# Performance work log

Measured on AMD Instinct MI355X. Metric: run time of the kernel, lower is better.

## Reference

```python
import math
import jax, jax.numpy as jnp
import numpy as np

B, N, E, H, DPOS = 64, 196, 768, 16, 3
DH = E // H


def rel_pos(num_patches):
    # deterministic relative-position encodings [N, N, 3] = (dx, dy, d^2)
    v = int(math.isqrt(num_patches))
    ind = jnp.arange(v)[None, :] - jnp.arange(v)[:, None]          # [v, v]
    indx = jnp.tile(ind, (v, v))                                    # [N, N]
    indy = jnp.repeat(jnp.repeat(ind, v, axis=0), v, axis=1)       # [N, N]
    indd = indx ** 2 + indy ** 2
    return jnp.stack([indx, indy, indd], axis=-1).astype(jnp.float32)


def setup_inputs() -> dict:
    key = jax.random.key(0)
    ks = jax.random.split(key, 9)
    std = 0.02  # trunc_normal std used by the module's init
    return {
        "q": jax.random.normal(ks[0], (B, N, E), jnp.float32),
        "k": jax.random.normal(ks[1], (B, N, E), jnp.float32),
        "v": jax.random.normal(ks[2], (B, N, E), jnp.float32),
        "mask": jnp.ones((B, 1, N, N), jnp.bool_),
        "Wq": jax.random.normal(ks[3], (E, E), jnp.float32) * std,
        "Wk": jax.random.normal(ks[4], (E, E), jnp.float32) * std,
        "Wv": jax.random.normal(ks[5], (E, E), jnp.float32) * std,
        "Wo": jax.random.normal(ks[6], (E, E), jnp.float32) * std,
        "bo": jnp.zeros((E,), jnp.float32),
        "Wpos": jax.random.normal(ks[7], (H, DPOS), jnp.float32) * std,
        "bpos": jnp.zeros((H,), jnp.float32),
        "gating": jnp.ones((H,), jnp.float32),
    }


def reference(q, k, v, mask, Wq, Wk, Wv, Wo, bo, Wpos, bpos, gating):
    b, n, _ = q.shape

    def heads(x, W):  # [b, n, E] -> [b, H, n, DH]
        return (x @ W.T).reshape(b, n, H, DH).transpose(0, 2, 1, 3)

    Q, K, V = heads(q, Wq), heads(k, Wk), heads(v, Wv)

    energy = jnp.einsum('bhqd,bhkd->bhqk', Q, K) / math.sqrt(DH)
    energy = jnp.where(mask, energy, -jnp.inf)
    content = jax.nn.softmax(energy, axis=-1)                      # [b, H, n, n]

    rel = rel_pos(n)                                               # [n, n, 3]
    pos = jnp.einsum('qkp,hp->hqk', rel, Wpos) + bpos[:, None, None]
    pos = jax.nn.softmax(pos, axis=-1)[None]                       # [1, H, n, n]

    g = jax.nn.sigmoid(gating)[None, :, None, None]
    score = (1.0 - g) * content + g * pos
    score = score / jnp.sum(score, axis=-1, keepdims=True)

    attn = jnp.einsum('bhqk,bhkd->bhqd', score, V)
    out = attn.transpose(0, 2, 1, 3).reshape(b, n, E) @ Wo.T + bo
    return out
```

## Files before the change

kernel.cpp:

```cpp
#include <hip/hip_runtime.h>
#include <hip/hip_bf16.h>

#define BB 64
#define NN 196
#define EE 768
#define HH 16
#define DHH 48

typedef short bf16x8 __attribute__((ext_vector_type(8)));
typedef float f32x4 __attribute__((ext_vector_type(4)));
typedef unsigned short u16;
typedef unsigned short u16x8 __attribute__((ext_vector_type(8)));
typedef unsigned int u32;

static __device__ __forceinline__ u16 f2bf(float f) {
  union { float f; u32 u; } un; un.f = f;
  u32 u = un.u;
  u32 r = (u + 0x7fffu + ((u >> 16) & 1u)) >> 16;
  return (u16)r;
}

static __device__ __forceinline__ u16 f2bf_hw(float f) {
  __hip_bfloat16 h = __float2bfloat16(f);
  return __builtin_bit_cast(u16, h);
}

#define GLOAD16(GP, LP)                                                        \
  __builtin_amdgcn_global_load_lds(                                            \
      (const __attribute__((address_space(1))) void*)(GP),                     \
      (__attribute__((address_space(3))) void*)(LP), 16, 0, 0)

static __device__ __forceinline__ int xcd_swz(int bid, int nwg) {
  int q = nwg >> 3, r = nwg & 7;
  int xcd = bid & 7, i = bid >> 3;
  return (xcd < r ? xcd * (q + 1) : r * (q + 1) + (xcd - r) * q) + i;
}

__global__ __launch_bounds__(64) void pos_kernel(const float* __restrict__ Wpos,
                                                 const float* __restrict__ bpos,
                                                 float* __restrict__ pos) {
  int bid = blockIdx.x;
  int h = bid / NN, q = bid % NN;
  int lane = threadIdx.x;
  float w0 = Wpos[h * 3 + 0], w1 = Wpos[h * 3 + 1], w2 = Wpos[h * 3 + 2];
  float bb = bpos[h];
  int qx = q % 14, qy = q / 14;
  float e[4];
  float mx = -1e30f;
#pragma unroll
  for (int i = 0; i < 4; ++i) {
    int k = lane + 64 * i;
    float val = -1e30f;
    if (k < NN) {
      int kx = k % 14, ky = k / 14;
      float dx = (float)(kx - qx), dy = (float)(ky - qy);
      val = w0 * dx + w1 * dy + w2 * (dx * dx + dy * dy) + bb;
    }
    e[i] = val;
    mx = fmaxf(mx, val);
  }
#pragma unroll
  for (int off = 1; off < 64; off <<= 1) mx = fmaxf(mx, __shfl_xor(mx, off));
  float s = 0.f;
#pragma unroll
  for (int i = 0; i < 4; ++i) {
    int k = lane + 64 * i;
    float p = (k < NN) ? expf(e[i] - mx) : 0.f;
    e[i] = p;
    s += p;
  }
#pragma unroll
  for (int off = 1; off < 64; off <<= 1) s += __shfl_xor(s, off);
  float inv = 1.f / s;
#pragma unroll
  for (int i = 0; i < 4; ++i) {
    int k = lane + 64 * i;
    if (k < NN) pos[(size_t)h * NN * NN + (size_t)q * NN + k] = e[i] * inv;
  }
}

__global__ __launch_bounds__(256) void cvtw_kernel(const float* __restrict__ W0,
                                                   const float* __restrict__ W1,
                                                   const float* __restrict__ W2,
                                                   const float* __restrict__ W3,
                                                   u16* __restrict__ out) {
  const float* Ws[4] = {W0, W1, W2, W3};
  int mat = blockIdx.y;
  const float* src = Ws[mat];
  int idx = blockIdx.x * 256 + threadIdx.x;
  float4 f = ((const float4*)src)[idx];
  short4 s;
  s.x = (short)f2bf_hw(f.x);
  s.y = (short)f2bf_hw(f.y);
  s.z = (short)f2bf_hw(f.z);
  s.w = (short)f2bf_hw(f.w);
  *(short4*)(out + (size_t)mat * EE * EE + (size_t)idx * 4) = s;
}

__global__ __launch_bounds__(256) void cvtx_kernel(const float* __restrict__ q,
                                                   const float* __restrict__ k,
                                                   const float* __restrict__ v,
                                                   u16* __restrict__ qb,
                                                   u16* __restrict__ kb,
                                                   u16* __restrict__ vb) {
  const float* srcs[3] = {q, k, v};
  u16* dsts[3] = {qb, kb, vb};
  const float* src = srcs[blockIdx.y];
  u16* dst = dsts[blockIdx.y];
#pragma unroll
  for (int c = 0; c < 4; ++c) {
    size_t idx = (size_t)blockIdx.x * 1024 + c * 256 + threadIdx.x;
    float4 f = ((const float4*)src)[idx];
    short4 s;
    s.x = (short)f2bf_hw(f.x);
    s.y = (short)f2bf_hw(f.y);
    s.z = (short)f2bf_hw(f.z);
    s.w = (short)f2bf_hw(f.w);
    ((short4*)dst)[idx] = s;
  }
}

template <bool OUT_F32>
static __device__ __forceinline__ void gemm_body(const u16* __restrict__ Aptr,
                                                 const u16* __restrict__ Wb,
                                                 void* __restrict__ Yptr,
                                                 const float* __restrict__ bias,
                                                 int m0, int n0) {
  __shared__ u16 As[3][128 * 32];
  __shared__ u16 Bs[3][128 * 32];
  const int tid = threadIdx.x;
  const int lane = tid & 63, wid = tid >> 6;
  const int wm = wid >> 1, wn = wid & 1;
  const int r16 = lane & 15, g4 = lane >> 4;
  f32x4 acc[4][4];
#pragma unroll
  for (int i = 0; i < 4; ++i)
#pragma unroll
    for (int j = 0; j < 4; ++j) acc[i][j] = (f32x4){0.f, 0.f, 0.f, 0.f};

  auto gloadA = [&](int b, int k0) {
#pragma unroll
    for (int c = 0; c < 2; ++c) {
      int s = c * 256 + tid;
      GLOAD16(Aptr + (size_t)(m0 + (s >> 2)) * EE + k0 + (s & 3) * 8,
              &As[b][s * 8]);
    }
  };
  auto gloadB = [&](int b, int k0) {
#pragma unroll
    for (int c = 0; c < 2; ++c) {
      int s = c * 256 + tid;
      GLOAD16(Wb + (size_t)(n0 + (s >> 2)) * EE + k0 + (s & 3) * 8,
              &Bs[b][s * 8]);
    }
  };

  gloadA(0, 0);  gloadB(0, 0);
  gloadA(1, 32); gloadB(1, 32);
  asm volatile("s_waitcnt vmcnt(4)" ::: "memory");
  asm volatile("s_barrier" ::: "memory");

  for (int t = 0; t < 24; ++t) {
    const int cb = t % 3;
    const int sb = (t + 2) % 3;
    const bool st = t < 22;
    if (st) {
      gloadA(sb, (t + 2) * 32);
      gloadB(sb, (t + 2) * 32);
    }
    bf16x8 af[4], bf[4];
#pragma unroll
    for (int i = 0; i < 4; ++i)
      af[i] = *(const bf16x8*)&As[cb][(wm * 64 + i * 16 + r16) * 32 + g4 * 8];
#pragma unroll
    for (int j = 0; j < 4; ++j)
      bf[j] = *(const bf16x8*)&Bs[cb][(wn * 64 + j * 16 + r16) * 32 + g4 * 8];
#pragma unroll
    for (int i = 0; i < 4; ++i)
#pragma unroll
      for (int j = 0; j < 4; ++j)
        acc[i][j] = __builtin_amdgcn_mfma_f32_16x16x32_bf16(af[i], bf[j], acc[i][j], 0, 0, 0);
    if (st)
      asm volatile("s_waitcnt vmcnt(4)" ::: "memory");
    else
      asm volatile("s_waitcnt vmcnt(0)" ::: "memory");
    asm volatile("s_barrier" ::: "memory");
  }

#pragma unroll
  for (int i = 0; i < 4; ++i) {
    int row = m0 + wm * 64 + i * 16 + g4 * 4;
#pragma unroll
    for (int j = 0; j < 4; ++j) {
      int col = n0 + wn * 64 + j * 16 + r16;
#pragma unroll
      for (int v = 0; v < 4; ++v) {
        float val = acc[i][j][v];
        if (OUT_F32)
          ((float*)Yptr)[(size_t)(row + v) * EE + col] = val + bias[col];
        else
          ((u16*)Yptr)[(size_t)(row + v) * EE + col] = f2bf(val);
      }
    }
  }
}

__global__ __launch_bounds__(256) void qkv_gemm(const u16* __restrict__ qb,
                                                const u16* __restrict__ kb,
                                                const u16* __restrict__ vb,
                                                const u16* __restrict__ Wqb,
                                                const u16* __restrict__ Wkb,
                                                const u16* __restrict__ Wvb,
                                                u16* __restrict__ Qp,
                                                u16* __restrict__ Kp,
                                                u16* __restrict__ Vp) {
  int sid = xcd_swz(blockIdx.x, 3 * 98 * 6);
  int z = sid / 588, rem = sid % 588;
  int m0 = (rem / 6) * 128, n0 = (rem % 6) * 128;
  const u16* A = (z == 0) ? qb : (z == 1) ? kb : vb;
  const u16* W = (z == 0) ? Wqb : (z == 1) ? Wkb : Wvb;
  u16* Y = (z == 0) ? Qp : (z == 1) ? Kp : Vp;
  gemm_body<false>(A, W, Y, nullptr, m0, n0);
}

__global__ __launch_bounds__(256) void out_gemm(const u16* __restrict__ ctx,
                                                const u16* __restrict__ Wob,
                                                float* __restrict__ out,
                                                const float* __restrict__ bo) {
  int sid = xcd_swz(blockIdx.x, 98 * 6);
  int m0 = (sid / 6) * 128, n0 = (sid % 6) * 128;
  gemm_body<true>(ctx, Wob, out, bo, m0, n0);
}

__global__ __launch_bounds__(512) void attn_kernel(const u16* __restrict__ Qp,
                                                   const u16* __restrict__ Kp,
                                                   const u16* __restrict__ Vp,
                                                   const float* __restrict__ pos,
                                                   const float* __restrict__ gating,
                                                   u16* __restrict__ ctx) {
  __shared__ u16 Qs[208 * 72];
  __shared__ u16 Ks[208 * 72];
  __shared__ u16 Vt[48 * 232];
  __shared__ u16 sc[8][16 * 232];
  int bh = blockIdx.x;
  int b = bh >> 4, h = bh & 15;
  int tid = threadIdx.x;
  {
    u32* z = (u32*)&Qs[0];
    for (int i = tid; i < (208 * 72) / 2; i += 512) z[i] = 0u;
    z = (u32*)&Ks[0];
    for (int i = tid; i < (208 * 72) / 2; i += 512) z[i] = 0u;
    z = (u32*)&Vt[0];
    for (int i = tid; i < (48 * 232) / 2; i += 512) z[i] = 0u;
  }
  __syncthreads();
  const u16* Qb = Qp + (size_t)b * NN * EE + h * DHH;
  const u16* Kb = Kp + (size_t)b * NN * EE + h * DHH;
  const u16* Vb = Vp + (size_t)b * NN * EE + h * DHH;
  for (int c = tid; c < NN * 12; c += 512) {
    int row = c / 12, k4 = (c % 12) * 4;
    short4 v = *(const short4*)(Qb + (size_t)row * EE + k4);
    *(short4*)&Qs[row * 72 + k4] = v;
  }
  for (int c = tid; c < NN * 12; c += 512) {
    int row = c / 12, k4 = (c % 12) * 4;
    short4 v = *(const short4*)(Kb + (size_t)row * EE + k4);
    *(short4*)&Ks[row * 72 + k4] = v;
  }
  for (int c = tid; c < NN * 12; c += 512) {
    int key = c / 12, d4 = (c % 12) * 4;
    short4 v = *(const short4*)(Vb + (size_t)key * EE + d4);
    Vt[(d4 + 0) * 232 + key] = (u16)v.x;
    Vt[(d4 + 1) * 232 + key] = (u16)v.y;
    Vt[(d4 + 2) * 232 + key] = (u16)v.z;
    Vt[(d4 + 3) * 232 + key] = (u16)v.w;
  }
  __syncthreads();

  int wid = tid >> 6, lane = tid & 63;
  int r16 = lane & 15, g4 = lane >> 4;
  float g = 1.f / (1.f + expf(-gating[h]));
  float omg = 1.f - g;
  u16* scw = &sc[wid][0];
  const float scale = 0.14433756729740643f;
  const float* posh = pos + (size_t)h * NN * NN;

  for (int rt = wid; rt < 13; rt += 8) {
    int q0 = rt * 16;
    bf16x8 aQ0 = *(const bf16x8*)&Qs[(q0 + r16) * 72 + g4 * 8];
    bf16x8 aQ1 = *(const bf16x8*)&Qs[(q0 + r16) * 72 + 32 + g4 * 8];
    f32x4 e[13];
#pragma unroll
    for (int ct = 0; ct < 13; ++ct) {
      bf16x8 b0 = *(const bf16x8*)&Ks[(ct * 16 + r16) * 72 + g4 * 8];
      bf16x8 b1 = *(const bf16x8*)&Ks[(ct * 16 + r16) * 72 + 32 + g4 * 8];
      f32x4 t = (f32x4){0.f, 0.f, 0.f, 0.f};
      t = __builtin_amdgcn_mfma_f32_16x16x32_bf16(aQ0, b0, t, 0, 0, 0);
      t = __builtin_amdgcn_mfma_f32_16x16x32_bf16(aQ1, b1, t, 0, 0, 0);
      e[ct] = t;
    }
    float mx[4] = {-1e30f, -1e30f, -1e30f, -1e30f};
#pragma unroll
    for (int ct = 0; ct < 13; ++ct) {
      int cix = ct * 16 + r16;
      bool valid = cix < NN;
#pragma unroll
      for (int v = 0; v < 4; ++v) {
        float ev = e[ct][v] * scale;
        ev = valid ? ev : -1e30f;
        e[ct][v] = ev;
        mx[v] = fmaxf(mx[v], ev);
      }
    }
#pragma unroll
    for (int v = 0; v < 4; ++v)
#pragma unroll
      for (int off = 1; off < 16; off <<= 1) mx[v] = fmaxf(mx[v], __shfl_xor(mx[v], off));
    float sm[4] = {0.f, 0.f, 0.f, 0.f};
#pragma unroll
    for (int ct = 0; ct < 13; ++ct)
#pragma unroll
      for (int v = 0; v < 4; ++v) {
        float p = __expf(e[ct][v] - mx[v]);
        e[ct][v] = p;
        sm[v] += p;
      }
#pragma unroll
    for (int v = 0; v < 4; ++v)
#pragma unroll
      for (int off = 1; off < 16; off <<= 1) sm[v] += __shfl_xor(sm[v], off);
    float inv[4];
#pragma unroll
    for (int v = 0; v < 4; ++v) inv[v] = 1.f / sm[v];
    int qg[4];
#pragma unroll
    for (int v = 0; v < 4; ++v) qg[v] = q0 + g4 * 4 + v;
    float t2[4] = {0.f, 0.f, 0.f, 0.f};
#pragma unroll
    for (int ct = 0; ct < 13; ++ct) {
      int cix = ct * 16 + r16;
      bool valid = cix < NN;
#pragma unroll
      for (int v = 0; v < 4; ++v) {
        float content = e[ct][v] * inv[v];
        float pv = 0.f;
        if (valid && qg[v] < NN) pv = posh[(size_t)qg[v] * NN + cix];
        float s = omg * content + g * pv;
        e[ct][v] = s;
        t2[v] += s;
      }
    }
#pragma unroll
    for (int v = 0; v < 4; ++v)
#pragma unroll
      for (int off = 1; off < 16; off <<= 1) t2[v] += __shfl_xor(t2[v], off);
    float inv2[4];
#pragma unroll
    for (int v = 0; v < 4; ++v) inv2[v] = 1.f / t2[v];
#pragma unroll
    for (int ct = 0; ct < 14; ++ct)
#pragma unroll
      for (int v = 0; v < 4; ++v) {
        float s = (ct < 13) ? e[ct][v] * inv2[v] : 0.f;
        scw[(g4 * 4 + v) * 232 + ct * 16 + r16] = f2bf(s);
      }
    asm volatile("s_waitcnt lgkmcnt(0)" ::: "memory");
#pragma unroll
    for (int dt = 0; dt < 3; ++dt) {
      f32x4 pv = (f32x4){0.f, 0.f, 0.f, 0.f};
#pragma unroll
      for (int kt = 0; kt < 7; ++kt) {
        bf16x8 aS = *(const bf16x8*)&scw[r16 * 232 + kt * 32 + g4 * 8];
        bf16x8 bV = *(const bf16x8*)&Vt[(dt * 16 + r16) * 232 + kt * 32 + g4 * 8];
        pv = __builtin_amdgcn_mfma_f32_16x16x32_bf16(aS, bV, pv, 0, 0, 0);
      }
#pragma unroll
      for (int v = 0; v < 4; ++v) {
        if (qg[v] < NN)
          ctx[((size_t)b * NN + qg[v]) * EE + h * DHH + dt * 16 + r16] = f2bf(pv[v]);
      }
    }
  }
}

extern "C" void kernel_launch(void* const* d_in, const int* in_sizes, int n_in,
                              void* d_out, int out_size, void* d_ws, size_t ws_size,
                              hipStream_t stream) {
  const float* q = (const float*)d_in[0];
  const float* k = (const float*)d_in[1];
  const float* v = (const float*)d_in[2];
  const float* Wq = (const float*)d_in[4];
  const float* Wk = (const float*)d_in[5];
  const float* Wv = (const float*)d_in[6];
  const float* Wo = (const float*)d_in[7];
  const float* bo = (const float*)d_in[8];
  const float* Wpos = (const float*)d_in[9];
  const float* bpos = (const float*)d_in[10];
  const float* gating = (const float*)d_in[11];
  float* out = (float*)d_out;

  char* ws = (char*)d_ws;
  const size_t elems = (size_t)BB * NN * EE;
  u16* Qp = (u16*)ws;
  u16* Kp = Qp + elems;
  u16* Vp = Kp + elems;
  u16* ctx = Vp + elems;
  float* pos = (float*)(ws + 4 * elems * sizeof(u16));
  u16* Wqb = (u16*)(ws + 4 * elems * sizeof(u16) + (size_t)HH * NN * NN * sizeof(float));
  u16* Wkb = Wqb + (size_t)EE * EE;
  u16* Wvb = Wkb + (size_t)EE * EE;
  u16* Wob = Wvb + (size_t)EE * EE;
  u16* qb = (u16*)d_out;
  u16* kb = qb + elems;
  u16* vb = ctx;

  hipLaunchKernelGGL(pos_kernel, dim3(HH * NN), dim3(64), 0, stream, Wpos, bpos, pos);
  hipLaunchKernelGGL(cvtw_kernel, dim3(EE * EE / 4 / 256, 4), dim3(256), 0, stream,
                     Wq, Wk, Wv, Wo, Wqb);
  hipLaunchKernelGGL(cvtx_kernel, dim3(2352, 3), dim3(256), 0, stream,
                     q, k, v, qb, kb, vb);

  hipLaunchKernelGGL(qkv_gemm, dim3(3 * 98 * 6), dim3(256), 0, stream,
                     qb, kb, vb, Wqb, Wkb, Wvb, Qp, Kp, Vp);

  hipLaunchKernelGGL(attn_kernel, dim3(BB * HH), dim3(512), 0, stream,
                     Qp, Kp, Vp, pos, gating, ctx);

  hipLaunchKernelGGL(out_gemm, dim3(98 * 6), dim3(256), 0, stream,
                     ctx, Wob, out, bo);
}
```

Baseline: 222.8 us.

## Restructure attention kernel to 256 threads, register-resident Q, and drop renormalization

The attention kernel moves from 512 to 256 threads per block with launch bounds allowing two blocks per CU. Q fragments now load straight from global memory into registers, so the Q shared-memory tile and its zeroing go away and each block uses less LDS. The second row-sum normalization is removed on the reasoning that the mixed score already sums to one, and the omg factor is folded into the softmax reciprocal. Score rows are converted with the hardware bf16 conversion and the S fragments are loaded once and reused across the three V tiles. Each wave now handles up to four row tiles, so the block runs longer and register pressure rises.

```diff
diff --git a/kernel.cpp b/kernel.cpp
--- a/kernel.cpp
+++ b/kernel.cpp
@@ -232,42 +232,51 @@
   gemm_body<true>(ctx, Wob, out, bo, m0, n0);
 }
 
-__global__ __launch_bounds__(512) void attn_kernel(const u16* __restrict__ Qp,
-                                                   const u16* __restrict__ Kp,
-                                                   const u16* __restrict__ Vp,
-                                                   const float* __restrict__ pos,
-                                                   const float* __restrict__ gating,
-                                                   u16* __restrict__ ctx) {
-  __shared__ u16 Qs[208 * 72];
+__global__ __launch_bounds__(256, 2) void attn_kernel(const u16* __restrict__ Qp,
+                                                      const u16* __restrict__ Kp,
+                                                      const u16* __restrict__ Vp,
+                                                      const float* __restrict__ pos,
+                                                      const float* __restrict__ gating,
+                                                      u16* __restrict__ ctx) {
   __shared__ u16 Ks[208 * 72];
   __shared__ u16 Vt[48 * 232];
-  __shared__ u16 sc[8][16 * 232];
+  __shared__ u16 sc[4][16 * 224];
   int bh = blockIdx.x;
   int b = bh >> 4, h = bh & 15;
   int tid = threadIdx.x;
-  {
-    u32* z = (u32*)&Qs[0];
-    for (int i = tid; i < (208 * 72) / 2; i += 512) z[i] = 0u;
-    z = (u32*)&Ks[0];
-    for (int i = tid; i < (208 * 72) / 2; i += 512) z[i] = 0u;
-    z = (u32*)&Vt[0];
-    for (int i = tid; i < (48 * 232) / 2; i += 512) z[i] = 0u;
-  }
-  __syncthreads();
+  int wid = tid >> 6, lane = tid & 63;
+  int r16 = lane & 15, g4 = lane >> 4;
+
   const u16* Qb = Qp + (size_t)b * NN * EE + h * DHH;
   const u16* Kb = Kp + (size_t)b * NN * EE + h * DHH;
   const u16* Vb = Vp + (size_t)b * NN * EE + h * DHH;
-  for (int c = tid; c < NN * 12; c += 512) {
-    int row = c / 12, k4 = (c % 12) * 4;
-    short4 v = *(const short4*)(Qb + (size_t)row * EE + k4);
-    *(short4*)&Qs[row * 72 + k4] = v;
-  }
-  for (int c = tid; c < NN * 12; c += 512) {
+
+  bf16x8 aQ0[4], aQ1[4];
+#pragma unroll
+  for (int i = 0; i < 4; ++i) {
+    int rt = wid + 4 * i;
+    if (rt < 13) {
+      int qrow = rt * 16 + r16;
+      if (qrow > NN - 1) qrow = NN - 1;
+      const u16* qp = Qb + (size_t)qrow * EE;
+      aQ0[i] = *(const bf16x8*)(qp + g4 * 8);
+      aQ1[i] = *(const bf16x8*)(qp + 32 + g4 * 8);
+    }
+  }
+
+  {
+    u32* z = (u32*)&Ks[0];
+    for (int i = tid; i < (208 * 72) / 2; i += 256) z[i] = 0u;
+    z = (u32*)&Vt[0];
+    for (int i = tid; i < (48 * 232) / 2; i += 256) z[i] = 0u;
+  }
+  __syncthreads();
+  for (int c = tid; c < NN * 12; c += 256) {
     int row = c / 12, k4 = (c % 12) * 4;
     short4 v = *(const short4*)(Kb + (size_t)row * EE + k4);
     *(short4*)&Ks[row * 72 + k4] = v;
   }
-  for (int c = tid; c < NN * 12; c += 512) {
+  for (int c = tid; c < NN * 12; c += 256) {
     int key = c / 12, d4 = (c % 12) * 4;
     short4 v = *(const short4*)(Vb + (size_t)key * EE + d4);
     Vt[(d4 + 0) * 232 + key] = (u16)v.x;
@@ -277,107 +286,95 @@
   }
   __syncthreads();
 
-  int wid = tid >> 6, lane = tid & 63;
-  int r16 = lane & 15, g4 = lane >> 4;
   float g = 1.f / (1.f + expf(-gating[h]));
   float omg = 1.f - g;
   u16* scw = &sc[wid][0];
   const float scale = 0.14433756729740643f;
   const float* posh = pos + (size_t)h * NN * NN;
 
-  for (int rt = wid; rt < 13; rt += 8) {
-    int q0 = rt * 16;
-    bf16x8 aQ0 = *(const bf16x8*)&Qs[(q0 + r16) * 72 + g4 * 8];
-    bf16x8 aQ1 = *(const bf16x8*)&Qs[(q0 + r16) * 72 + 32 + g4 * 8];
-    f32x4 e[13];
-#pragma unroll
-    for (int ct = 0; ct < 13; ++ct) {
-      bf16x8 b0 = *(const bf16x8*)&Ks[(ct * 16 + r16) * 72 + g4 * 8];
-      bf16x8 b1 = *(const bf16x8*)&Ks[(ct * 16 + r16) * 72 + 32 + g4 * 8];
-      f32x4 t = (f32x4){0.f, 0.f, 0.f, 0.f};
-      t = __builtin_amdgcn_mfma_f32_16x16x32_bf16(aQ0, b0, t, 0, 0, 0);
-      t = __builtin_amdgcn_mfma_f32_16x16x32_bf16(aQ1, b1, t, 0, 0, 0);
-      e[ct] = t;
-    }
-    float mx[4] = {-1e30f, -1e30f, -1e30f, -1e30f};
-#pragma unroll
-    for (int ct = 0; ct < 13; ++ct) {
-      int cix = ct * 16 + r16;
-      bool valid = cix < NN;
+#pragma unroll
+  for (int i = 0; i < 4; ++i) {
+    int rt = wid + 4 * i;
+    if (rt < 13) {
+      int q0 = rt * 16;
+      f32x4 e[13];
+#pragma unroll
+      for (int ct = 0; ct < 13; ++ct) {
+        bf16x8 b0 = *(const bf16x8*)&Ks[(ct * 16 + r16) * 72 + g4 * 8];
+        bf16x8 b1 = *(const bf16x8*)&Ks[(ct * 16 + r16) * 72 + 32 + g4 * 8];
+        f32x4 t = (f32x4){0.f, 0.f, 0.f, 0.f};
+        t = __builtin_amdgcn_mfma_f32_16x16x32_bf16(aQ0[i], b0, t, 0, 0, 0);
+        t = __builtin_amdgcn_mfma_f32_16x16x32_bf16(aQ1[i], b1, t, 0, 0, 0);
+        e[ct] = t;
+      }
+      float mx[4] = {-1e30f, -1e30f, -1e30f, -1e30f};
+#pragma unroll
+      for (int ct = 0; ct < 13; ++ct) {
+        int cix = ct * 16 + r16;
+        bool valid = cix < NN;
+#pragma unroll
+        for (int v = 0; v < 4; ++v) {
+          float ev = e[ct][v] * scale;
+          ev = valid ? ev : -1e30f;
+          e[ct][v] = ev;
+          mx[v] = fmaxf(mx[v], ev);
+        }
+      }
+#pragma unroll
+      for (int v = 0; v < 4; ++v)
+#pragma unroll
+        for (int off = 1; off < 16; off <<= 1) mx[v] = fmaxf(mx[v], __shfl_xor(mx[v], off));
+      float sm[4] = {0.f, 0.f, 0.f, 0.f};
+#pragma unroll
+      for (int ct = 0; ct < 13; ++ct)
+#pragma unroll
+        for (int v = 0; v < 4; ++v) {
+          float p = __expf(e[ct][v] - mx[v]);
+          e[ct][v] = p;
+          sm[v] += p;
+        }
+#pragma unroll
+      for (int v = 0; v < 4; ++v)
+#pragma unroll
+        for (int off = 1; off < 16; off <<= 1) sm[v] += __shfl_xor(sm[v], off);
+      float oinv[4];
+      int qg[4];
 #pragma unroll
       for (int v = 0; v < 4; ++v) {
-        float ev = e[ct][v] * scale;
-        ev = valid ? ev : -1e30f;
-        e[ct][v] = ev;
-        mx[v] = fmaxf(mx[v], ev);
+        oinv[v] = omg / sm[v];
+        qg[v] = q0 + g4 * 4 + v;
       }
-    }
-#pragma unroll
-    for (int v = 0; v < 4; ++v)
-#pragma unroll
-      for (int off = 1; off < 16; off <<= 1) mx[v] = fmaxf(mx[v], __shfl_xor(mx[v], off));
-    float sm[4] = {0.f, 0.f, 0.f, 0.f};
-#pragma unroll
-    for (int ct = 0; ct < 13; ++ct)
-#pragma unroll
-      for (int v = 0; v < 4; ++v) {
-        float p = __expf(e[ct][v] - mx[v]);
-        e[ct][v] = p;
-        sm[v] += p;
-      }
-#pragma unroll
-    for (int v = 0; v < 4; ++v)
-#pragma unroll
-      for (int off = 1; off < 16; off <<= 1) sm[v] += __shfl_xor(sm[v], off);
-    float inv[4];
-#pragma unroll
-    for (int v = 0; v < 4; ++v) inv[v] = 1.f / sm[v];
-    int qg[4];
-#pragma unroll
-    for (int v = 0; v < 4; ++v) qg[v] = q0 + g4 * 4 + v;
-    float t2[4] = {0.f, 0.f, 0.f, 0.f};
-#pragma unroll
-    for (int ct = 0; ct < 13; ++ct) {
-      int cix = ct * 16 + r16;
-      bool valid = cix < NN;
-#pragma unroll
-      for (int v = 0; v < 4; ++v) {
-        float content = e[ct][v] * inv[v];
-        float pv = 0.f;
-        if (valid && qg[v] < NN) pv = posh[(size_t)qg[v] * NN + cix];
-        float s = omg * content + g * pv;
-        e[ct][v] = s;
-        t2[v] += s;
-      }
-    }
-#pragma unroll
-    for (int v = 0; v < 4; ++v)
-#pragma unroll
-      for (int off = 1; off < 16; off <<= 1) t2[v] += __shfl_xor(t2[v], off);
-    float inv2[4];
-#pragma unroll
-    for (int v = 0; v < 4; ++v) inv2[v] = 1.f / t2[v];
-#pragma unroll
-    for (int ct = 0; ct < 14; ++ct)
-#pragma unroll
-      for (int v = 0; v < 4; ++v) {
-        float s = (ct < 13) ? e[ct][v] * inv2[v] : 0.f;
-        scw[(g4 * 4 + v) * 232 + ct * 16 + r16] = f2bf(s);
-      }
-    asm volatile("s_waitcnt lgkmcnt(0)" ::: "memory");
-#pragma unroll
-    for (int dt = 0; dt < 3; ++dt) {
-      f32x4 pv = (f32x4){0.f, 0.f, 0.f, 0.f};
-#pragma unroll
-      for (int kt = 0; kt < 7; ++kt) {
-        bf16x8 aS = *(const bf16x8*)&scw[r16 * 232 + kt * 32 + g4 * 8];
-        bf16x8 bV = *(const bf16x8*)&Vt[(dt * 16 + r16) * 232 + kt * 32 + g4 * 8];
-        pv = __builtin_amdgcn_mfma_f32_16x16x32_bf16(aS, bV, pv, 0, 0, 0);
-      }
-#pragma unroll
-      for (int v = 0; v < 4; ++v) {
-        if (qg[v] < NN)
-          ctx[((size_t)b * NN + qg[v]) * EE + h * DHH + dt * 16 + r16] = f2bf(pv[v]);
+#pragma unroll
+      for (int ct = 0; ct < 14; ++ct)
+#pragma unroll
+        for (int v = 0; v < 4; ++v) {
+          float s = 0.f;
+          if (ct < 13) {
+            int cix = ct * 16 + r16;
+            float pv = 0.f;
+            if (cix < NN && qg[v] < NN) pv = posh[(size_t)qg[v] * NN + cix];
+            s = e[ct][v] * oinv[v] + g * pv;
+          }
+          scw[(g4 * 4 + v) * 224 + ct * 16 + r16] = f2bf_hw(s);
+        }
+      asm volatile("s_waitcnt lgkmcnt(0)" ::: "memory");
+      bf16x8 aS[7];
+#pragma unroll
+      for (int kt = 0; kt < 7; ++kt)
+        aS[kt] = *(const bf16x8*)&scw[r16 * 224 + kt * 32 + g4 * 8];
+#pragma unroll
+      for (int dt = 0; dt < 3; ++dt) {
+        f32x4 pv = (f32x4){0.f, 0.f, 0.f, 0.f};
+#pragma unroll
+        for (int kt = 0; kt < 7; ++kt) {
+          bf16x8 bV = *(const bf16x8*)&Vt[(dt * 16 + r16) * 232 + kt * 32 + g4 * 8];
+          pv = __builtin_amdgcn_mfma_f32_16x16x32_bf16(aS[kt], bV, pv, 0, 0, 0);
+        }
+#pragma unroll
+        for (int v = 0; v < 4; ++v) {
+          if (qg[v] < NN)
+            ctx[((size_t)b * NN + qg[v]) * EE + h * DHH + dt * 16 + r16] = f2bf(pv[v]);
+        }
       }
     }
   }
@@ -423,7 +420,7 @@
   hipLaunchKernelGGL(qkv_gemm, dim3(3 * 98 * 6), dim3(256), 0, stream,
                      qb, kb, vb, Wqb, Wkb, Wvb, Qp, Kp, Vp);
 
-  hipLaunchKernelGGL(attn_kernel, dim3(BB * HH), dim3(512), 0, stream,
+  hipLaunchKernelGGL(attn_kernel, dim3(BB * HH), dim3(256), 0, stream,
                      Qp, Kp, Vp, pos, gating, ctx);
 
   hipLaunchKernelGGL(out_gemm, dim3(98 * 6), dim3(256), 0, stream,
```

Result: slower. 288.5 us (+29.5%).
